# Optimization experiments

Measured on AMD Instinct MI355X. Metric: run time of the kernel, lower is better.

Reference implementation:

```python
import jax, jax.numpy as jnp
import numpy as np

N_NODES = 100000
N_EDGES = 1600000
F_IN = 128
HID = 128


def setup_inputs() -> dict:
    key = jax.random.key(0)
    ks = jax.random.split(key, 10)
    x = jax.random.normal(ks[0], (N_NODES, F_IN), dtype=jnp.float32)
    edge_index = jax.random.randint(ks[1], (2, N_EDGES), 0, N_NODES, dtype=jnp.int64)
    edge_weight = jax.random.uniform(ks[2], (N_EDGES,), dtype=jnp.float32)
    # Glorot-style params for the three GCNConv layers (conv_mid reused twice)
    W_in = jax.random.normal(ks[3], (F_IN, HID), dtype=jnp.float32) / np.sqrt(F_IN)
    b_in = jnp.zeros((HID,), dtype=jnp.float32)
    W_mid = jax.random.normal(ks[4], (HID, HID), dtype=jnp.float32) / np.sqrt(HID)
    b_mid = jnp.zeros((HID,), dtype=jnp.float32)
    W_fin = jax.random.normal(ks[5], (HID, 1), dtype=jnp.float32) / np.sqrt(HID)
    b_fin = jnp.zeros((1,), dtype=jnp.float32)
    return {"x": x, "edge_index": edge_index, "edge_weight": edge_weight,
            "W_in": W_in, "b_in": b_in, "W_mid": W_mid, "b_mid": b_mid,
            "W_fin": W_fin, "b_fin": b_fin}


def _gcn_norm(edge_index, edge_weight, n_nodes):
    """PyG GCNConv normalization with implicit self-loops (weight 1).
    Returns (edge_norm [E], self_norm [N]) where self_norm = 1/deg."""
    dst = edge_index[1]
    deg = jax.ops.segment_sum(edge_weight, dst, num_segments=n_nodes) + 1.0
    dinv = jnp.where(deg > 0, jax.lax.rsqrt(deg), 0.0)  # deg^-1/2
    edge_norm = dinv[edge_index[0]] * edge_weight * dinv[dst]
    self_norm = dinv * dinv  # self-loop: dinv[i] * 1 * dinv[i]
    return edge_norm, self_norm


def _gcn_conv(x, edge_index, edge_norm, self_norm, W, b, n_nodes):
    h = x @ W  # [N, out]
    msgs = edge_norm[:, None] * h[edge_index[0]]  # [E, out]
    agg = jax.ops.segment_sum(msgs, edge_index[1], num_segments=n_nodes)
    return agg + self_norm[:, None] * h + b


def reference(x, edge_index, edge_weight, W_in, b_in, W_mid, b_mid, W_fin, b_fin):
    n = x.shape[0]
    edge_norm, self_norm = _gcn_norm(edge_index, edge_weight, n)
    h = jax.nn.relu(_gcn_conv(x, edge_index, edge_norm, self_norm, W_in, b_in, n))
    h = jax.nn.relu(_gcn_conv(h, edge_index, edge_norm, self_norm, W_mid, b_mid, n))
    h = jax.nn.relu(_gcn_conv(h, edge_index, edge_norm, self_norm, W_mid, b_mid, n))
    out = _gcn_conv(h, edge_index, edge_norm, self_norm, W_fin, b_fin, n)
    return out  # [N, 1]
```

## Files before the change

### kernel.cpp

```cpp
#include <hip/hip_runtime.h>
#include <stdint.h>

#define N_NODES 100000
#define N_EDGES 1600000
#define F 128
#define CBN 512
#define NCBK 196
#define CHUNK 4096
#define BUFCAP 10240

typedef _Float16 f16;
typedef _Float16 f16x4 __attribute__((ext_vector_type(4)));
typedef _Float16 f16x8 __attribute__((ext_vector_type(8)));
typedef float f32x4 __attribute__((ext_vector_type(4)));

__device__ inline float unpackw(unsigned int p) {
    unsigned short b = (unsigned short)(p & 0x7FFF);
    return (float)__builtin_bit_cast(f16, b);
}


__global__ void k_zero0(int* bktcnt) {
    int i = threadIdx.x;
    if (i < NCBK) bktcnt[i] = 0;
}

__launch_bounds__(256)
__global__ void k_bhist(const int* __restrict__ ei, int* __restrict__ bktcnt, int e) {
    __shared__ int h[NCBK];
    int tid = threadIdx.x;
    if (tid < NCBK) h[tid] = 0;
    __syncthreads();
    int base = blockIdx.x * CHUNK;
    int cnt = min(CHUNK, e - base);
    const int* dst = ei + N_EDGES + base;
    if (cnt == CHUNK) {
        const int4* d4 = (const int4*)dst;
#pragma unroll
        for (int k = 0; k < 4; k++) {
            int4 v = d4[tid + k * 256];
            atomicAdd(&h[v.x >> 9], 1);
            atomicAdd(&h[v.y >> 9], 1);
            atomicAdd(&h[v.z >> 9], 1);
            atomicAdd(&h[v.w >> 9], 1);
        }
    } else {
        for (int i = tid; i < cnt; i += 256)
            atomicAdd(&h[dst[i] >> 9], 1);
    }
    __syncthreads();
    if (tid < NCBK && h[tid]) atomicAdd(&bktcnt[tid], h[tid]);
}

__launch_bounds__(256)
__global__ void k_bktscan(const int* __restrict__ bktcnt, int* __restrict__ gbase,
                          int* __restrict__ gcur, int* __restrict__ row) {
    __shared__ int ls[256];
    int tid = threadIdx.x;
    int v = (tid < NCBK) ? bktcnt[tid] : 0;
    ls[tid] = v;
    __syncthreads();
    for (int off = 1; off < 256; off <<= 1) {
        int t = (tid >= off) ? ls[tid - off] : 0;
        __syncthreads();
        ls[tid] += t;
        __syncthreads();
    }
    int ex = ls[tid] - v;
    if (tid < NCBK) { gbase[tid] = ex; gcur[tid] = ex; }
    if (tid == NCBK) gbase[NCBK] = N_EDGES;
    if (tid == 0) row[N_NODES] = N_EDGES;
}


__launch_bounds__(256)
__global__ void k_binA(const int* __restrict__ ei, const float* __restrict__ w,
                       int* __restrict__ gcur, int2* __restrict__ stage, int e) {
    __shared__ int hist[256];
    __shared__ int bst[257];
    __shared__ int gb[256];
    __shared__ int ls[256];
    __shared__ int rec[CHUNK];
    __shared__ int meta[CHUNK];
    int tid = threadIdx.x;
    int base = blockIdx.x * CHUNK;
    int cnt = min(CHUNK, e - base);
    hist[tid] = 0;
    __syncthreads();

    int ew_[16], mr_[16];
    int nloc = 0;
    if (cnt == CHUNK) {
#pragma unroll
        for (int k = 0; k < 16; k++) {
            int i = base + tid + k * 256;
            int s = ei[i];
            int d = ei[N_EDGES + i];
            f16 hw = (f16)w[i];
            unsigned short wb = __builtin_bit_cast(unsigned short, hw);
            ew_[k] = (int)(((unsigned int)s << 15) | (wb & 0x7FFF));
            int cb = d >> 9;
            int local = d & (CBN - 1);
            int r = atomicAdd(&hist[cb], 1);
            mr_[k] = (cb << 22) | (local << 13) | r;
        }
        nloc = 16;
    } else {
        for (int i = tid; i < cnt; i += 256) {
            int s = ei[base + i];
            int d = ei[N_EDGES + base + i];
            f16 hw = (f16)w[base + i];
            unsigned short wb = __builtin_bit_cast(unsigned short, hw);
            ew_[nloc] = (int)(((unsigned int)s << 15) | (wb & 0x7FFF));
            int cb = d >> 9;
            int local = d & (CBN - 1);
            int r = atomicAdd(&hist[cb], 1);
            mr_[nloc] = (cb << 22) | (local << 13) | r;
            nloc++;
        }
    }
    __syncthreads();
    int v = hist[tid];
    ls[tid] = v;
    __syncthreads();
    for (int off = 1; off < 256; off <<= 1) {
        int t = (tid >= off) ? ls[tid - off] : 0;
        __syncthreads();
        ls[tid] += t;
        __syncthreads();
    }
    bst[tid] = ls[tid] - v;
    if (tid == 255) bst[256] = ls[255];
    __syncthreads();
    for (int k = 0; k < nloc; k++) {
        int m = mr_[k];
        int cb = m >> 22;
        int pos = bst[cb] + (m & 0x1FFF);
        rec[pos] = ew_[k];
        meta[pos] = (cb << 9) | ((m >> 13) & 0x1FF);
    }
    __syncthreads();
    if (tid < NCBK) {
        int c = bst[tid + 1] - bst[tid];
        gb[tid] = c ? atomicAdd(&gcur[tid], c) : 0;
    }
    __syncthreads();
    for (int j = tid; j < cnt; j += 256) {
        int m = meta[j];
        int cb = m >> 9;
        stage[gb[cb] + (j - bst[cb])] = make_int2(m & 511, rec[j]);
    }
}

__launch_bounds__(256)
__global__ void k_binB(const int2* __restrict__ stage, const int* __restrict__ gbase,
                       unsigned int* __restrict__ edges, int* __restrict__ row,
                       float* __restrict__ dinv) {
    __shared__ int cnt[CBN];
    __shared__ int ex[CBN + 1];
    __shared__ int cur[CBN];
    __shared__ int ls[256];
    __shared__ unsigned int buf[BUFCAP];
    int tid = threadIdx.x;
    int cb = blockIdx.x;
    int n0 = cb * CBN;
    int nn = min(CBN, N_NODES - n0);
    int base = gbase[cb];
    int hi = gbase[cb + 1];
    cnt[tid] = 0;
    cnt[tid + 256] = 0;
    __syncthreads();
    for (int j = base + tid; j < hi; j += 256)
        atomicAdd(&cnt[stage[j].x], 1);
    __syncthreads();
    int a = cnt[2 * tid], b = cnt[2 * tid + 1];
    int s = a + b;
    ls[tid] = s;
    __syncthreads();
    for (int off = 1; off < 256; off <<= 1) {
        int t = (tid >= off) ? ls[tid - off] : 0;
        __syncthreads();
        ls[tid] += t;
        __syncthreads();
    }
    int bx = ls[tid] - s;
    ex[2 * tid] = bx;
    ex[2 * tid + 1] = bx + a;
    cur[2 * tid] = bx;
    cur[2 * tid + 1] = bx + a;
    if (tid == 255) ex[512] = ls[255];
    __syncthreads();
    for (int l = tid; l < nn; l += 256) row[n0 + l] = base + ex[l];
    for (int j = base + tid; j < hi; j += 256) {
        int2 r = stage[j];
        int p = atomicAdd(&cur[r.x], 1);
        buf[p] = (unsigned int)r.y;
    }
    __syncthreads();
    int range = hi - base;
    for (int j = tid; j < range; j += 256)
        edges[base + j] = buf[j];
    for (int l = tid; l < nn; l += 256) {
        int lo = ex[l];
        int h2 = ex[l + 1];
        float sm = 1.0f;
        for (int j = lo; j < h2; j++) sm += unpackw(buf[j]);
        dinv[n0 + l] = rsqrtf(sm);
    }
}


__global__ void k_cvt(const float* __restrict__ X, f16* __restrict__ Y, int n8) {
    int i = blockIdx.x * blockDim.x + threadIdx.x;
    if (i < n8) {
        float4 a = ((const float4*)X)[i * 2];
        float4 b = ((const float4*)X)[i * 2 + 1];
        f16x8 o;
        o[0] = (f16)a.x; o[1] = (f16)a.y; o[2] = (f16)a.z; o[3] = (f16)a.w;
        o[4] = (f16)b.x; o[5] = (f16)b.y; o[6] = (f16)b.z; o[7] = (f16)b.w;
        ((f16x8*)Y)[i] = o;
    }
}

__global__ void k_wt2(const float* __restrict__ Wa, const float* __restrict__ Wb,
                      f16* __restrict__ Wta, f16* __restrict__ Wtb) {
    const float* W = blockIdx.x ? Wb : Wa;
    f16* Wt = blockIdx.x ? Wtb : Wta;
    int t = threadIdx.x;
#pragma unroll
    for (int it = 0; it < 64; it++) {
        int idx = t + it * 256;
        int k = idx >> 7, n = idx & 127;
        Wt[n * 128 + k] = (f16)W[idx];
    }
}


#define LDK 136

__launch_bounds__(256, 2)
__global__ void k_gemm16(const f16* __restrict__ A, const f16* __restrict__ Wt,
                         const float* __restrict__ dinv, f16* __restrict__ H, int nrows) {
    __shared__ f16 Ws[128 * LDK];
    int tid = threadIdx.x;
    int r0 = blockIdx.x * 128;
    int wave = tid >> 6;
    int lane = tid & 63;
    int lrow = lane & 15;
    int quad = lane >> 4;

    f16x8 a[2][4];
#pragma unroll
    for (int mt = 0; mt < 2; mt++) {
        int row = r0 + wave * 32 + mt * 16 + lrow;
#pragma unroll
        for (int kc = 0; kc < 4; kc++) {
            if (row < nrows)
                a[mt][kc] = *(const f16x8*)&A[(size_t)row * F + kc * 32 + quad * 8];
            else
                a[mt][kc] = (f16x8){};
        }
    }
#pragma unroll
    for (int it = 0; it < 8; it++) {
        int c = tid + it * 256;
        int rw = c >> 4;
        int off = (c & 15) * 8;
        *(f16x8*)&Ws[rw * LDK + off] = *(const f16x8*)&Wt[rw * 128 + off];
    }
    __syncthreads();

    f32x4 acc[2][8] = {};
#pragma unroll
    for (int kc = 0; kc < 4; kc++) {
        f16x8 b[8];
#pragma unroll
        for (int nt = 0; nt < 8; nt++)
            b[nt] = *(const f16x8*)&Ws[(nt * 16 + lrow) * LDK + kc * 32 + quad * 8];
#pragma unroll
        for (int nt = 0; nt < 8; nt++) {
            acc[0][nt] = __builtin_amdgcn_mfma_f32_16x16x32_f16(a[0][kc], b[nt], acc[0][nt], 0, 0, 0);
            acc[1][nt] = __builtin_amdgcn_mfma_f32_16x16x32_f16(a[1][kc], b[nt], acc[1][nt], 0, 0, 0);
        }
    }
    __syncthreads();
#pragma unroll
    for (int mt = 0; mt < 2; mt++) {
#pragma unroll
        for (int r = 0; r < 4; r++) {
            int lr = wave * 32 + mt * 16 + quad * 4 + r;
            int grow = r0 + lr;
            float dv = (grow < nrows) ? dinv[grow] : 0.f;
#pragma unroll
            for (int nt = 0; nt < 8; nt++)
                Ws[lr * 132 + nt * 16 + lrow] = (f16)(acc[mt][nt][r] * dv);
        }
    }
    __syncthreads();
#pragma unroll
    for (int it = 0; it < 8; it++) {
        int c = it * 256 + tid;
        int rw = c >> 4;
        int col = (c & 15) * 8;
        int grow = r0 + rw;
        if (grow < nrows)
            *(f16x8*)&H[(size_t)grow * F + col] = *(const f16x8*)&Ws[rw * 132 + col];
    }
}


__launch_bounds__(256)
__global__ void k_agg(const f16* __restrict__ H16, const int* __restrict__ row,
                      const unsigned int* __restrict__ edges,
                      const float* __restrict__ dinv, const float* __restrict__ bias,
                      f16* __restrict__ out, int n) {
    int node = blockIdx.x * 4 + (threadIdx.x >> 6);
    if (node >= n) return;
    int lane = threadIdx.x & 63;
    int qq = lane >> 4;
    int sub = lane & 15;
    float acc[8] = {0.f, 0.f, 0.f, 0.f, 0.f, 0.f, 0.f, 0.f};
    float acc2[8] = {0.f, 0.f, 0.f, 0.f, 0.f, 0.f, 0.f, 0.f};
    int beg = row[node], end = row[node + 1];
    int deg = end - beg;
    int t = qq;
    for (; t + 4 < deg; t += 8) {
        unsigned int e0 = edges[beg + t];
        unsigned int e1 = edges[beg + t + 4];
        float w0 = unpackw(e0);
        float w1 = unpackw(e1);
        f16x8 v0 = *(const f16x8*)&H16[(size_t)(e0 >> 15) * F + sub * 8];
        f16x8 v1 = *(const f16x8*)&H16[(size_t)(e1 >> 15) * F + sub * 8];
#pragma unroll
        for (int j = 0; j < 8; j++) {
            acc[j] = fmaf(w0, (float)v0[j], acc[j]);
            acc2[j] = fmaf(w1, (float)v1[j], acc2[j]);
        }
    }
    for (; t < deg; t += 4) {
        unsigned int e0 = edges[beg + t];
        float w0 = unpackw(e0);
        f16x8 v0 = *(const f16x8*)&H16[(size_t)(e0 >> 15) * F + sub * 8];
#pragma unroll
        for (int j = 0; j < 8; j++)
            acc[j] = fmaf(w0, (float)v0[j], acc[j]);
    }
#pragma unroll
    for (int j = 0; j < 8; j++) {
        acc[j] += acc2[j];
        acc[j] += __shfl_xor(acc[j], 16, 64);
        acc[j] += __shfl_xor(acc[j], 32, 64);
    }
    if (lane < 16) {
        float dd = dinv[node];
        f16x8 h = *(const f16x8*)&H16[(size_t)node * F + lane * 8];
        float4 b0 = *(const float4*)&bias[lane * 8];
        float4 b1 = *(const float4*)&bias[lane * 8 + 4];
        float bb[8] = {b0.x, b0.y, b0.z, b0.w, b1.x, b1.y, b1.z, b1.w};
        f16x8 o;
#pragma unroll
        for (int j = 0; j < 8; j++) {
            float r = fmaxf(fmaf(dd, acc[j] + (float)h[j], bb[j]), 0.f);
            o[j] = (f16)r;
        }
        *(f16x8*)&out[(size_t)node * F + lane * 8] = o;
    }
}

__launch_bounds__(256)
__global__ void k_agg_dot(const f16* __restrict__ H16, const int* __restrict__ row,
                          const unsigned int* __restrict__ edges,
                          const float* __restrict__ dinv, const float* __restrict__ bias,
                          const float* __restrict__ Wf, float* __restrict__ sout, int n) {
    int node = blockIdx.x * 4 + (threadIdx.x >> 6);
    if (node >= n) return;
    int lane = threadIdx.x & 63;
    int qq = lane >> 4;
    int sub = lane & 15;
    float acc[8] = {0.f, 0.f, 0.f, 0.f, 0.f, 0.f, 0.f, 0.f};
    float acc2[8] = {0.f, 0.f, 0.f, 0.f, 0.f, 0.f, 0.f, 0.f};
    int beg = row[node], end = row[node + 1];
    int deg = end - beg;
    int t = qq;
    for (; t + 4 < deg; t += 8) {
        unsigned int e0 = edges[beg + t];
        unsigned int e1 = edges[beg + t + 4];
        float w0 = unpackw(e0);
        float w1 = unpackw(e1);
        f16x8 v0 = *(const f16x8*)&H16[(size_t)(e0 >> 15) * F + sub * 8];
        f16x8 v1 = *(const f16x8*)&H16[(size_t)(e1 >> 15) * F + sub * 8];
#pragma unroll
        for (int j = 0; j < 8; j++) {
            acc[j] = fmaf(w0, (float)v0[j], acc[j]);
            acc2[j] = fmaf(w1, (float)v1[j], acc2[j]);
        }
    }
    for (; t < deg; t += 4) {
        unsigned int e0 = edges[beg + t];
        float w0 = unpackw(e0);
        f16x8 v0 = *(const f16x8*)&H16[(size_t)(e0 >> 15) * F + sub * 8];
#pragma unroll
        for (int j = 0; j < 8; j++)
            acc[j] = fmaf(w0, (float)v0[j], acc[j]);
    }
#pragma unroll
    for (int j = 0; j < 8; j++) {
        acc[j] += acc2[j];
        acc[j] += __shfl_xor(acc[j], 16, 64);
        acc[j] += __shfl_xor(acc[j], 32, 64);
    }
    if (lane < 16) {
        float dd = dinv[node];
        f16x8 h = *(const f16x8*)&H16[(size_t)node * F + lane * 8];
        float4 b0 = *(const float4*)&bias[lane * 8];
        float4 b1 = *(const float4*)&bias[lane * 8 + 4];
        float bb[8] = {b0.x, b0.y, b0.z, b0.w, b1.x, b1.y, b1.z, b1.w};
        float4 w0 = *(const float4*)&Wf[lane * 8];
        float4 w1 = *(const float4*)&Wf[lane * 8 + 4];
        float ww[8] = {w0.x, w0.y, w0.z, w0.w, w1.x, w1.y, w1.z, w1.w};
        float p = 0.f;
#pragma unroll
        for (int j = 0; j < 8; j++)
            p += fmaxf(fmaf(dd, acc[j] + (float)h[j], bb[j]), 0.f) * ww[j];
        p += __shfl_xor(p, 8, 64);
        p += __shfl_xor(p, 4, 64);
        p += __shfl_xor(p, 2, 64);
        p += __shfl_xor(p, 1, 64);
        if (lane == 0) sout[node] = dd * p;
    }
}

__global__ void k_aggs(const float* __restrict__ s, const int* __restrict__ row,
                       const unsigned int* __restrict__ edges,
                       const float* __restrict__ dinv, const float* __restrict__ bf,
                       float* __restrict__ out, int n) {
    int i = blockIdx.x * blockDim.x + threadIdx.x;
    if (i >= n) return;
    float dd = dinv[i];
    float ae = s[i];
    int beg = row[i], end = row[i + 1];
    for (int j = beg; j < end; j++) {
        unsigned int p = edges[j];
        ae = fmaf(unpackw(p), s[p >> 15], ae);
    }
    out[i] = fmaf(dd, ae, bf[0]);
}


extern "C" void kernel_launch(void* const* d_in, const int* in_sizes, int n_in,
                              void* d_out, int out_size, void* d_ws, size_t ws_size,
                              hipStream_t stream) {
    const float* x    = (const float*)d_in[0];
    const int*   ei   = (const int*)d_in[1];
    const float* ew   = (const float*)d_in[2];
    const float* Win  = (const float*)d_in[3];
    const float* bin  = (const float*)d_in[4];
    const float* Wmid = (const float*)d_in[5];
    const float* bmid = (const float*)d_in[6];
    const float* Wfin = (const float*)d_in[7];
    const float* bfin = (const float*)d_in[8];
    float* out = (float*)d_out;

    char* ws = (char*)d_ws;
    size_t off = 0;
    auto alloc = [&](size_t bytes) -> char* {
        char* p = ws + off;
        off = (off + bytes + 255) & ~(size_t)255;
        return p;
    };
    float* dinv  = (float*)alloc((size_t)N_NODES * 4);
    int*   row   = (int*)alloc((size_t)(N_NODES + 1) * 4);
    unsigned int* edges = (unsigned int*)alloc((size_t)N_EDGES * 4);
    int*   bktcnt = (int*)alloc(256 * 4);
    int*   gbase  = (int*)alloc(256 * 4);
    int*   gcur   = (int*)alloc(256 * 4);
    f16*   wtin  = (f16*)alloc(128 * 128 * 2);
    f16*   wtmid = (f16*)alloc(128 * 128 * 2);
    f16*   H16   = (f16*)alloc((size_t)N_NODES * F * 2);
    f16*   AB16  = (f16*)alloc((size_t)N_NODES * F * 2);
    int2* stage = (int2*)H16;
    float* sbuf = (float*)AB16;

    dim3 b256(256);
    int gN = (N_NODES + 255) / 256;
    int gW = (N_NODES + 3) / 4;
    int gG = (N_NODES + 127) / 128;
    int n8 = N_NODES * F / 8;
    int gC = (n8 + 255) / 256;
    int gA = (N_EDGES + CHUNK - 1) / CHUNK;

    hipLaunchKernelGGL(k_zero0, dim3(1), b256, 0, stream, bktcnt);
    hipLaunchKernelGGL(k_bhist, dim3(gA), b256, 0, stream, ei, bktcnt, N_EDGES);
    hipLaunchKernelGGL(k_bktscan, dim3(1), b256, 0, stream, bktcnt, gbase, gcur, row);
    hipLaunchKernelGGL(k_binA, dim3(gA), b256, 0, stream, ei, ew, gcur, stage, N_EDGES);
    hipLaunchKernelGGL(k_binB, dim3(NCBK), b256, 0, stream, stage, gbase, edges, row, dinv);
    hipLaunchKernelGGL(k_cvt, dim3(gC), b256, 0, stream, x, AB16, n8);
    hipLaunchKernelGGL(k_wt2, dim3(2), b256, 0, stream, Win, Wmid, wtin, wtmid);

    hipLaunchKernelGGL(k_gemm16, dim3(gG), b256, 0, stream, AB16, wtin, dinv, H16, N_NODES);
    hipLaunchKernelGGL(k_agg, dim3(gW), b256, 0, stream, H16, row, edges, dinv, bin, AB16, N_NODES);
    hipLaunchKernelGGL(k_gemm16, dim3(gG), b256, 0, stream, AB16, wtmid, dinv, H16, N_NODES);
    hipLaunchKernelGGL(k_agg, dim3(gW), b256, 0, stream, H16, row, edges, dinv, bmid, AB16, N_NODES);
    hipLaunchKernelGGL(k_gemm16, dim3(gG), b256, 0, stream, AB16, wtmid, dinv, H16, N_NODES);
    hipLaunchKernelGGL(k_agg_dot, dim3(gW), b256, 0, stream, H16, row, edges, dinv, bmid, Wfin, sbuf, N_NODES);
    hipLaunchKernelGGL(k_aggs, dim3(gN), b256, 0, stream, sbuf, row, edges, dinv, bfin, out, N_NODES);
}
```

Before: 421.5 us.

## Map each node to 16 lanes and unroll edge gather by four

The aggregation kernels now assign one 16-lane group per node instead of a full 64-lane wave, and each thread walks all of the node's edges with four independent gathers per iteration, using clamped indices and zeroed weights for the tail. This removes the cross-quarter shuffle reduction and the lane-predicated epilogue, and puts more loads in flight per thread. In exchange there is less parallelism per node and more sensitivity to degree imbalance within a wave, plus some redundant loads in the tail.

```diff
diff --git a/kernel.cpp b/kernel.cpp
--- a/kernel.cpp
+++ b/kernel.cpp
@@ -314,57 +314,48 @@
                       const unsigned int* __restrict__ edges,
                       const float* __restrict__ dinv, const float* __restrict__ bias,
                       f16* __restrict__ out, int n) {
-    int node = blockIdx.x * 4 + (threadIdx.x >> 6);
+    int node = blockIdx.x * 16 + (threadIdx.x >> 4);
     if (node >= n) return;
-    int lane = threadIdx.x & 63;
-    int qq = lane >> 4;
-    int sub = lane & 15;
-    float acc[8] = {0.f, 0.f, 0.f, 0.f, 0.f, 0.f, 0.f, 0.f};
-    float acc2[8] = {0.f, 0.f, 0.f, 0.f, 0.f, 0.f, 0.f, 0.f};
+    int sub = threadIdx.x & 15;
     int beg = row[node], end = row[node + 1];
-    int deg = end - beg;
-    int t = qq;
-    for (; t + 4 < deg; t += 8) {
-        unsigned int e0 = edges[beg + t];
-        unsigned int e1 = edges[beg + t + 4];
+    float acc0[8] = {}, acc1[8] = {}, acc2[8] = {}, acc3[8] = {};
+    int em1 = end - 1;
+    for (int t = beg; t < end; t += 4) {
+        int i1 = min(t + 1, em1);
+        int i2 = min(t + 2, em1);
+        int i3 = min(t + 3, em1);
+        unsigned int e0 = edges[t];
+        unsigned int e1 = edges[i1];
+        unsigned int e2 = edges[i2];
+        unsigned int e3 = edges[i3];
         float w0 = unpackw(e0);
-        float w1 = unpackw(e1);
+        float w1 = (t + 1 < end) ? unpackw(e1) : 0.f;
+        float w2 = (t + 2 < end) ? unpackw(e2) : 0.f;
+        float w3 = (t + 3 < end) ? unpackw(e3) : 0.f;
         f16x8 v0 = *(const f16x8*)&H16[(size_t)(e0 >> 15) * F + sub * 8];
         f16x8 v1 = *(const f16x8*)&H16[(size_t)(e1 >> 15) * F + sub * 8];
+        f16x8 v2 = *(const f16x8*)&H16[(size_t)(e2 >> 15) * F + sub * 8];
+        f16x8 v3 = *(const f16x8*)&H16[(size_t)(e3 >> 15) * F + sub * 8];
 #pragma unroll
         for (int j = 0; j < 8; j++) {
-            acc[j] = fmaf(w0, (float)v0[j], acc[j]);
-            acc2[j] = fmaf(w1, (float)v1[j], acc2[j]);
-        }
-    }
-    for (; t < deg; t += 4) {
-        unsigned int e0 = edges[beg + t];
-        float w0 = unpackw(e0);
-        f16x8 v0 = *(const f16x8*)&H16[(size_t)(e0 >> 15) * F + sub * 8];
-#pragma unroll
-        for (int j = 0; j < 8; j++)
-            acc[j] = fmaf(w0, (float)v0[j], acc[j]);
-    }
+            acc0[j] = fmaf(w0, (float)v0[j], acc0[j]);
+            acc1[j] = fmaf(w1, (float)v1[j], acc1[j]);
+            acc2[j] = fmaf(w2, (float)v2[j], acc2[j]);
+            acc3[j] = fmaf(w3, (float)v3[j], acc3[j]);
+        }
+    }
+    float dd = dinv[node];
+    f16x8 h = *(const f16x8*)&H16[(size_t)node * F + sub * 8];
+    float4 b0 = *(const float4*)&bias[sub * 8];
+    float4 b1 = *(const float4*)&bias[sub * 8 + 4];
+    float bb[8] = {b0.x, b0.y, b0.z, b0.w, b1.x, b1.y, b1.z, b1.w};
+    f16x8 o;
 #pragma unroll
     for (int j = 0; j < 8; j++) {
-        acc[j] += acc2[j];
-        acc[j] += __shfl_xor(acc[j], 16, 64);
-        acc[j] += __shfl_xor(acc[j], 32, 64);
-    }
-    if (lane < 16) {
-        float dd = dinv[node];
-        f16x8 h = *(const f16x8*)&H16[(size_t)node * F + lane * 8];
-        float4 b0 = *(const float4*)&bias[lane * 8];
-        float4 b1 = *(const float4*)&bias[lane * 8 + 4];
-        float bb[8] = {b0.x, b0.y, b0.z, b0.w, b1.x, b1.y, b1.z, b1.w};
-        f16x8 o;
-#pragma unroll
-        for (int j = 0; j < 8; j++) {
-            float r = fmaxf(fmaf(dd, acc[j] + (float)h[j], bb[j]), 0.f);
-            o[j] = (f16)r;
-        }
-        *(f16x8*)&out[(size_t)node * F + lane * 8] = o;
-    }
+        float a = acc0[j] + acc1[j] + acc2[j] + acc3[j] + (float)h[j];
+        o[j] = (f16)fmaxf(fmaf(dd, a, bb[j]), 0.f);
+    }
+    *(f16x8*)&out[(size_t)node * F + sub * 8] = o;
 }
 
 __launch_bounds__(256)
@@ -372,62 +363,55 @@
                           const unsigned int* __restrict__ edges,
                           const float* __restrict__ dinv, const float* __restrict__ bias,
                           const float* __restrict__ Wf, float* __restrict__ sout, int n) {
-    int node = blockIdx.x * 4 + (threadIdx.x >> 6);
+    int node = blockIdx.x * 16 + (threadIdx.x >> 4);
     if (node >= n) return;
-    int lane = threadIdx.x & 63;
-    int qq = lane >> 4;
-    int sub = lane & 15;
-    float acc[8] = {0.f, 0.f, 0.f, 0.f, 0.f, 0.f, 0.f, 0.f};
-    float acc2[8] = {0.f, 0.f, 0.f, 0.f, 0.f, 0.f, 0.f, 0.f};
+    int sub = threadIdx.x & 15;
     int beg = row[node], end = row[node + 1];
-    int deg = end - beg;
-    int t = qq;
-    for (; t + 4 < deg; t += 8) {
-        unsigned int e0 = edges[beg + t];
-        unsigned int e1 = edges[beg + t + 4];
+    float acc0[8] = {}, acc1[8] = {}, acc2[8] = {}, acc3[8] = {};
+    int em1 = end - 1;
+    for (int t = beg; t < end; t += 4) {
+        int i1 = min(t + 1, em1);
+        int i2 = min(t + 2, em1);
+        int i3 = min(t + 3, em1);
+        unsigned int e0 = edges[t];
+        unsigned int e1 = edges[i1];
+        unsigned int e2 = edges[i2];
+        unsigned int e3 = edges[i3];
         float w0 = unpackw(e0);
-        float w1 = unpackw(e1);
+        float w1 = (t + 1 < end) ? unpackw(e1) : 0.f;
+        float w2 = (t + 2 < end) ? unpackw(e2) : 0.f;
+        float w3 = (t + 3 < end) ? unpackw(e3) : 0.f;
         f16x8 v0 = *(const f16x8*)&H16[(size_t)(e0 >> 15) * F + sub * 8];
         f16x8 v1 = *(const f16x8*)&H16[(size_t)(e1 >> 15) * F + sub * 8];
+        f16x8 v2 = *(const f16x8*)&H16[(size_t)(e2 >> 15) * F + sub * 8];
+        f16x8 v3 = *(const f16x8*)&H16[(size_t)(e3 >> 15) * F + sub * 8];
 #pragma unroll
         for (int j = 0; j < 8; j++) {
-            acc[j] = fmaf(w0, (float)v0[j], acc[j]);
-            acc2[j] = fmaf(w1, (float)v1[j], acc2[j]);
-        }
-    }
-    for (; t < deg; t += 4) {
-        unsigned int e0 = edges[beg + t];
-        float w0 = unpackw(e0);
-        f16x8 v0 = *(const f16x8*)&H16[(size_t)(e0 >> 15) * F + sub * 8];
-#pragma unroll
-        for (int j = 0; j < 8; j++)
-            acc[j] = fmaf(w0, (float)v0[j], acc[j]);
-    }
+            acc0[j] = fmaf(w0, (float)v0[j], acc0[j]);
+            acc1[j] = fmaf(w1, (float)v1[j], acc1[j]);
+            acc2[j] = fmaf(w2, (float)v2[j], acc2[j]);
+            acc3[j] = fmaf(w3, (float)v3[j], acc3[j]);
+        }
+    }
+    float dd = dinv[node];
+    f16x8 h = *(const f16x8*)&H16[(size_t)node * F + sub * 8];
+    float4 b0 = *(const float4*)&bias[sub * 8];
+    float4 b1 = *(const float4*)&bias[sub * 8 + 4];
+    float bb[8] = {b0.x, b0.y, b0.z, b0.w, b1.x, b1.y, b1.z, b1.w};
+    float4 w0v = *(const float4*)&Wf[sub * 8];
+    float4 w1v = *(const float4*)&Wf[sub * 8 + 4];
+    float ww[8] = {w0v.x, w0v.y, w0v.z, w0v.w, w1v.x, w1v.y, w1v.z, w1v.w};
+    float p = 0.f;
 #pragma unroll
     for (int j = 0; j < 8; j++) {
-        acc[j] += acc2[j];
-        acc[j] += __shfl_xor(acc[j], 16, 64);
-        acc[j] += __shfl_xor(acc[j], 32, 64);
-    }
-    if (lane < 16) {
-        float dd = dinv[node];
-        f16x8 h = *(const f16x8*)&H16[(size_t)node * F + lane * 8];
-        float4 b0 = *(const float4*)&bias[lane * 8];
-        float4 b1 = *(const float4*)&bias[lane * 8 + 4];
-        float bb[8] = {b0.x, b0.y, b0.z, b0.w, b1.x, b1.y, b1.z, b1.w};
-        float4 w0 = *(const float4*)&Wf[lane * 8];
-        float4 w1 = *(const float4*)&Wf[lane * 8 + 4];
-        float ww[8] = {w0.x, w0.y, w0.z, w0.w, w1.x, w1.y, w1.z, w1.w};
-        float p = 0.f;
-#pragma unroll
-        for (int j = 0; j < 8; j++)
-            p += fmaxf(fmaf(dd, acc[j] + (float)h[j], bb[j]), 0.f) * ww[j];
-        p += __shfl_xor(p, 8, 64);
-        p += __shfl_xor(p, 4, 64);
-        p += __shfl_xor(p, 2, 64);
-        p += __shfl_xor(p, 1, 64);
-        if (lane == 0) sout[node] = dd * p;
-    }
+        float a = acc0[j] + acc1[j] + acc2[j] + acc3[j] + (float)h[j];
+        p += fmaxf(fmaf(dd, a, bb[j]), 0.f) * ww[j];
+    }
+    p += __shfl_xor(p, 8, 64);
+    p += __shfl_xor(p, 4, 64);
+    p += __shfl_xor(p, 2, 64);
+    p += __shfl_xor(p, 1, 64);
+    if (sub == 0) sout[node] = dd * p;
 }
 
 __global__ void k_aggs(const float* __restrict__ s, const int* __restrict__ row,
@@ -483,7 +467,7 @@
 
     dim3 b256(256);
     int gN = (N_NODES + 255) / 256;
-    int gW = (N_NODES + 3) / 4;
+    int gW = (N_NODES + 15) / 16;
     int gG = (N_NODES + 127) / 128;
     int n8 = N_NODES * F / 8;
     int gC = (n8 + 255) / 256;
```

New measurement: 408.6 us. 1.03x faster.
